# Kernel optimization log

Measured on AMD Instinct MI355X. Metric: run time of the kernel, lower is better.

The kernel has to match this reference:

```python
import jax, jax.numpy as jnp
import numpy as np


def setup_inputs() -> dict:
    key = jax.random.key(0)
    kq, ks, kr, kx, ky = jax.random.split(key, 5)
    B, C, H, W, K = 2, 64, 128, 256, 32
    Q = jax.random.normal(kq, (B, C, H, W), dtype=jnp.float32)
    S = jax.random.normal(ks, (B, C, H, W), dtype=jnp.float32)
    R = jax.random.normal(kr, (B, C, H, W), dtype=jnp.float32)
    Pos_x = jax.random.randint(kx, (H * W, K), 0, H, dtype=jnp.int64 if jax.config.jax_enable_x64 else jnp.int32)
    Pos_y = jax.random.randint(ky, (H * W, K), 0, W, dtype=jnp.int64 if jax.config.jax_enable_x64 else jnp.int32)
    return {"Q": Q, "S": S, "R": R, "Pos_x": Pos_x, "Pos_y": Pos_y}


def reference(Q, S, R, Pos_x, Pos_y):
    B, C, H, W = Q.shape
    N = H * W
    px = Pos_x.reshape(-1)  # [N*K]
    py = Pos_y.reshape(-1)
    K = px.shape[0] // N
    # Gather keys/values at candidate positions: [B, C, N*K] -> [B, C, N, K]
    Key = S[:, :, px, py].reshape(B, C, N, K)
    Value = R[:, :, px, py].reshape(B, C, N, K)
    # Queries: [B, N, C]
    Qf = Q.reshape(B, C, N).transpose(0, 2, 1)
    # Per-pixel scores over K candidates (NO 1/sqrt(d) scaling, as in original)
    score = jnp.einsum('bnc,bcnk->bnk', Qf, Key)
    attn = jax.nn.softmax(score, axis=-1)
    # Attention-weighted sum of values: [B, N, C]
    out = jnp.einsum('bnk,bcnk->bnc', attn, Value)
    return out.reshape(B, H, W, C).transpose(0, 3, 1, 2)
```

## Files before the change

### kernel.cpp

```cpp
#include <hip/hip_runtime.h>
#include <hip/hip_fp16.h>

constexpr int B = 2, C = 64, H = 128, W = 256, N = H * W, K = 32;

typedef _Float16 hf2 __attribute__((ext_vector_type(2)));

template <int CTRL>
__device__ __forceinline__ float dppf(float x) {
    int i = __builtin_bit_cast(int, x);
    int r = __builtin_amdgcn_update_dpp(i, i, CTRL, 0xF, 0xF, false);
    return __builtin_bit_cast(float, r);
}

__device__ __forceinline__ unsigned sel4(const ushort4& v, int g) {
    return g == 0 ? v.x : g == 1 ? v.y : g == 2 ? v.z : v.w;
}

__global__ __launch_bounds__(256) void fepam_prep(
    const float* __restrict__ Q, const float* __restrict__ S,
    const float* __restrict__ R,
    const int* __restrict__ Px, const int* __restrict__ Py,
    __half* __restrict__ Qt, __half* __restrict__ St, __half* __restrict__ Rt,
    unsigned short* __restrict__ Idx) {
    const int n0 = blockIdx.x * 64;
    const int b  = blockIdx.y;
    const int z  = blockIdx.z;

    if (z == 3) {
        if (b) return;
#pragma unroll
        for (int t = 0; t < 8; ++t) {
            const int e  = threadIdx.x + 256 * t;
            const int nl = e >> 5, k = e & 31;
            const int n  = n0 + nl;
            const int idx = Px[(size_t)n * K + k] * W + Py[(size_t)n * K + k];
            Idx[(size_t)n * K + (k & 7) * 4 + (k >> 3)] = (unsigned short)idx;
        }
        return;
    }

    __shared__ float tile[C][65];
    const float* src = (z == 0 ? S : (z == 1 ? R : Q)) + (size_t)b * C * N;
    __half2* d2 = (__half2*)((z == 0 ? St : (z == 1 ? Rt : Qt)) +
                             (size_t)b * N * C);
    {
        const int j = threadIdx.x & 63, c0 = threadIdx.x >> 6;
        const float* s = src + n0 + j;
#pragma unroll
        for (int r = 0; r < 16; ++r) {
            int c = c0 + r * 4;
            tile[c][j] = s[(size_t)c * N];
        }
    }
    __syncthreads();
    {
        const int c2 = threadIdx.x & 31, j0 = threadIdx.x >> 5;
#pragma unroll
        for (int r = 0; r < 8; ++r) {
            int j = j0 + 8 * r;
            d2[(size_t)(n0 + j) * 32 + c2] =
                __floats2half2_rn(tile[2 * c2][j], tile[2 * c2 + 1][j]);
        }
    }
}

__global__ __launch_bounds__(256, 6) void fepam_attn(
    const __half* __restrict__ Qt, const unsigned short* __restrict__ Idx,
    const __half* __restrict__ St, const __half* __restrict__ Rt,
    float* __restrict__ Out) {
    __shared__ __align__(16) float aw[32][32];
    __shared__ __align__(16) float ot[32][66];

    const int tid  = threadIdx.x;
    const int lane = tid & 63;
    const int wave = tid >> 6;
    const int bx   = blockIdx.x;
    const int b    = bx & 1;
    const int n0t  = (bx >> 1) * 32;
    const int n0   = n0t + wave * 8;

    const int c_oct = lane & 7;
    const int k_loc = lane >> 3;

    const __half* Qtb = Qt + (size_t)b * N * C;
    const __half* Stb = St + (size_t)b * N * C;
    const __half* Rtb = Rt + (size_t)b * N * C;

    auto ldi = [&](int p) {
        return *(const ushort4*)(Idx + (size_t)(n0 + p) * K + k_loc * 4);
    };

    {
        auto ldq = [&](int p) {
            return *(const float4*)(Qtb + (size_t)(n0 + p) * C + c_oct * 8);
        };
        auto ldk = [&](const ushort4& iv, int g) {
            return *(const float4*)(Stb + ((size_t)sel4(iv, g) << 6) +
                                    c_oct * 8);
        };

        ushort4 iv_c = ldi(0), iv_n = ldi(1);
        float4  q_c  = ldq(0), q_n  = ldq(1);
        float4  k_c[4];
#pragma unroll
        for (int g = 0; g < 4; ++g) k_c[g] = ldk(iv_c, g);

#pragma unroll
        for (int p = 0; p < 8; ++p) {
            float4 k_n[4];
            if (p < 7) {
#pragma unroll
                for (int g = 0; g < 4; ++g) k_n[g] = ldk(iv_n, g);
            }
            ushort4 iv_2;
            float4  q_2;
            if (p < 6) { iv_2 = ldi(p + 2); q_2 = ldq(p + 2); }

            float s[4];
#pragma unroll
            for (int g = 0; g < 4; ++g) {
                const hf2* k2 = (const hf2*)&k_c[g];
                const hf2* q2 = (const hf2*)&q_c;
                float acc = 0.f;
#pragma unroll
                for (int u = 0; u < 4; ++u)
                    acc = __builtin_amdgcn_fdot2(k2[u], q2[u], acc, false);
                s[g] = acc;
            }
#pragma unroll
            for (int g = 0; g < 4; ++g) {
                s[g] += dppf<0xB1>(s[g]);
                s[g] += dppf<0x4E>(s[g]);
                s[g] += dppf<0x141>(s[g]);
            }
            float m = fmaxf(fmaxf(s[0], s[1]), fmaxf(s[2], s[3]));
            m = fmaxf(m, dppf<0x128>(m));
            m = fmaxf(m, __shfl_xor(m, 16));
            m = fmaxf(m, __shfl_xor(m, 32));
            float e0 = __expf(s[0] - m), e1 = __expf(s[1] - m);
            float e2 = __expf(s[2] - m), e3 = __expf(s[3] - m);
            float l = (e0 + e1) + (e2 + e3);
            l += dppf<0x128>(l);
            l += __shfl_xor(l, 16);
            l += __shfl_xor(l, 32);
            const float inv = 1.0f / l;

            if (c_oct == 0) {
                *(float4*)&aw[wave * 8 + p][k_loc * 4] =
                    make_float4(e0 * inv, e1 * inv, e2 * inv, e3 * inv);
            }

#pragma unroll
            for (int g = 0; g < 4; ++g) k_c[g] = k_n[g];
            iv_c = iv_n; q_c = q_n;
            iv_n = iv_2; q_n = q_2;
        }
    }

    {
        const bool hi8  = (lane & 8)  != 0;
        const bool hi16 = (lane & 16) != 0;
        const bool hi32 = (lane & 32) != 0;

        auto ldv = [&](const ushort4& iv, int g) {
            return *(const float4*)(Rtb + ((size_t)sel4(iv, g) << 6) +
                                    c_oct * 8);
        };

        ushort4 i_c = ldi(0), i_n = ldi(1);
        float4  v_c[4];
#pragma unroll
        for (int g = 0; g < 4; ++g) v_c[g] = ldv(i_c, g);

#pragma unroll
        for (int p = 0; p < 8; ++p) {
            float4 v_n[4];
            if (p < 7) {
#pragma unroll
                for (int g = 0; g < 4; ++g) v_n[g] = ldv(i_n, g);
            }
            ushort4 i_2;
            if (p < 6) i_2 = ldi(p + 2);

            const float4 af = *(const float4*)&aw[wave * 8 + p][k_loc * 4];
            const float a[4] = {af.x, af.y, af.z, af.w};
            float acc[8] = {0, 0, 0, 0, 0, 0, 0, 0};
#pragma unroll
            for (int g = 0; g < 4; ++g) {
                const __half2* v2 = (const __half2*)&v_c[g];
#pragma unroll
                for (int u = 0; u < 4; ++u) {
                    const float2 vf = __half22float2(v2[u]);
                    acc[2 * u]     = fmaf(a[g], vf.x, acc[2 * u]);
                    acc[2 * u + 1] = fmaf(a[g], vf.y, acc[2 * u + 1]);
                }
            }

            float r4[4];
#pragma unroll
            for (int i = 0; i < 4; ++i) {
                const float send = hi8 ? acc[i] : acc[4 + i];
                const float recv = dppf<0x128>(send);
                r4[i] = (hi8 ? acc[4 + i] : acc[i]) + recv;
            }
            float r2[2];
#pragma unroll
            for (int i = 0; i < 2; ++i) {
                const float send = hi16 ? r4[i] : r4[2 + i];
                const float recv = __shfl_xor(send, 16);
                r2[i] = (hi16 ? r4[2 + i] : r4[i]) + recv;
            }
            {
                const float send = hi32 ? r2[0] : r2[1];
                const float recv = __shfl_xor(send, 32);
                const float r1   = (hi32 ? r2[1] : r2[0]) + recv;
                const int c = c_oct * 8 + (hi8 ? 4 : 0) + (hi16 ? 2 : 0) +
                              (hi32 ? 1 : 0);
                ot[wave * 8 + p][c] = r1;
            }

#pragma unroll
            for (int g = 0; g < 4; ++g) v_c[g] = v_n[g];
            i_c = i_n;
            i_n = i_2;
        }
    }
    __syncthreads();

    {
        const int j = tid & 31, c0 = tid >> 5;
        float* od = Out + (size_t)b * C * N + n0t + j;
#pragma unroll
        for (int r = 0; r < 8; ++r) {
            int c = c0 + r * 8;
            od[(size_t)c * N] = ot[j][c];
        }
    }
}

extern "C" void kernel_launch(void* const* d_in, const int* in_sizes, int n_in,
                              void* d_out, int out_size, void* d_ws, size_t ws_size,
                              hipStream_t stream) {
    const float* Q  = (const float*)d_in[0];
    const float* S  = (const float*)d_in[1];
    const float* R  = (const float*)d_in[2];
    const int*   Px = (const int*)d_in[3];
    const int*   Py = (const int*)d_in[4];
    float* Out = (float*)d_out;

    __half* St = (__half*)d_ws;
    __half* Rt = St + (size_t)B * N * C;
    __half* Qt = Rt + (size_t)B * N * C;
    unsigned short* Idx = (unsigned short*)(Qt + (size_t)B * N * C);

    dim3 pgrid(N / 64, B, 4);
    fepam_prep<<<pgrid, 256, 0, stream>>>(Q, S, R, Px, Py, Qt, St, Rt, Idx);

    dim3 ggrid(N / 32 * B);
    fepam_attn<<<ggrid, 256, 0, stream>>>(Qt, Idx, St, Rt, Out);
}
```

Before: 142.7 us.

## Split attention kernel into separate score and value-gather kernels

Splits the fused attention kernel into two launches. The first gathers keys and computes softmax weights, which it writes to a global fp16 buffer. The second gathers values and applies those weights. Each kernel touches only one gathered tensor (S or R), so the L2/MALL working set per phase is smaller and cache hit rates for the random gathers may improve. The cost is an extra launch, a global round trip for the weights (2*N*K fp16), and fp16 rounding of the attention weights.

Result: faster. 136.0 us (-4.7%).

```diff
diff --git a/kernel.cpp b/kernel.cpp
--- a/kernel.cpp
+++ b/kernel.cpp
@@ -64,11 +64,98 @@
     }
 }
 
-__global__ __launch_bounds__(256, 6) void fepam_attn(
+__global__ __launch_bounds__(256, 6) void fepam_scores(
     const __half* __restrict__ Qt, const unsigned short* __restrict__ Idx,
-    const __half* __restrict__ St, const __half* __restrict__ Rt,
-    float* __restrict__ Out) {
-    __shared__ __align__(16) float aw[32][32];
+    const __half* __restrict__ St, __half* __restrict__ AW) {
+    const int tid  = threadIdx.x;
+    const int lane = tid & 63;
+    const int wave = tid >> 6;
+    const int bx   = blockIdx.x;
+    const int b    = bx & 1;
+    const int n0   = (bx >> 1) * 32 + wave * 8;
+
+    const int c_oct = lane & 7;
+    const int k_loc = lane >> 3;
+
+    const __half* Qtb = Qt + (size_t)b * N * C;
+    const __half* Stb = St + (size_t)b * N * C;
+    __half* AWb = AW + (size_t)b * N * K;
+
+    auto ldi = [&](int p) {
+        return *(const ushort4*)(Idx + (size_t)(n0 + p) * K + k_loc * 4);
+    };
+    auto ldq = [&](int p) {
+        return *(const float4*)(Qtb + (size_t)(n0 + p) * C + c_oct * 8);
+    };
+    auto ldk = [&](const ushort4& iv, int g) {
+        return *(const float4*)(Stb + ((size_t)sel4(iv, g) << 6) + c_oct * 8);
+    };
+
+    ushort4 iv_c = ldi(0), iv_n = ldi(1);
+    float4  q_c  = ldq(0), q_n  = ldq(1);
+    float4  k_c[4];
+#pragma unroll
+    for (int g = 0; g < 4; ++g) k_c[g] = ldk(iv_c, g);
+
+#pragma unroll
+    for (int p = 0; p < 8; ++p) {
+        float4 k_n[4];
+        if (p < 7) {
+#pragma unroll
+            for (int g = 0; g < 4; ++g) k_n[g] = ldk(iv_n, g);
+        }
+        ushort4 iv_2;
+        float4  q_2;
+        if (p < 6) { iv_2 = ldi(p + 2); q_2 = ldq(p + 2); }
+
+        float s[4];
+#pragma unroll
+        for (int g = 0; g < 4; ++g) {
+            const hf2* k2 = (const hf2*)&k_c[g];
+            const hf2* q2 = (const hf2*)&q_c;
+            float acc = 0.f;
+#pragma unroll
+            for (int u = 0; u < 4; ++u)
+                acc = __builtin_amdgcn_fdot2(k2[u], q2[u], acc, false);
+            s[g] = acc;
+        }
+#pragma unroll
+        for (int g = 0; g < 4; ++g) {
+            s[g] += dppf<0xB1>(s[g]);
+            s[g] += dppf<0x4E>(s[g]);
+            s[g] += dppf<0x141>(s[g]);
+        }
+        float m = fmaxf(fmaxf(s[0], s[1]), fmaxf(s[2], s[3]));
+        m = fmaxf(m, dppf<0x128>(m));
+        m = fmaxf(m, __shfl_xor(m, 16));
+        m = fmaxf(m, __shfl_xor(m, 32));
+        float e0 = __expf(s[0] - m), e1 = __expf(s[1] - m);
+        float e2 = __expf(s[2] - m), e3 = __expf(s[3] - m);
+        float l = (e0 + e1) + (e2 + e3);
+        l += dppf<0x128>(l);
+        l += __shfl_xor(l, 16);
+        l += __shfl_xor(l, 32);
+        const float inv = 1.0f / l;
+
+        if (c_oct == 0) {
+            ushort4 hv;
+            hv.x = __half_as_ushort(__float2half_rn(e0 * inv));
+            hv.y = __half_as_ushort(__float2half_rn(e1 * inv));
+            hv.z = __half_as_ushort(__float2half_rn(e2 * inv));
+            hv.w = __half_as_ushort(__float2half_rn(e3 * inv));
+            *(ushort4*)(AWb + (size_t)(n0 + p) * K + k_loc * 4) = hv;
+        }
+
+#pragma unroll
+        for (int g = 0; g < 4; ++g) k_c[g] = k_n[g];
+        iv_c = iv_n; q_c = q_n;
+        iv_n = iv_2; q_n = q_2;
+    }
+}
+
+__global__ __launch_bounds__(256, 6) void fepam_values(
+    const unsigned short* __restrict__ Idx, const __half* __restrict__ AW,
+    const __half* __restrict__ Rt, float* __restrict__ Out) {
     __shared__ __align__(16) float ot[32][66];
 
     const int tid  = threadIdx.x;
@@ -81,149 +168,82 @@
 
     const int c_oct = lane & 7;
     const int k_loc = lane >> 3;
-
-    const __half* Qtb = Qt + (size_t)b * N * C;
-    const __half* Stb = St + (size_t)b * N * C;
+    const bool hi8  = (lane & 8)  != 0;
+    const bool hi16 = (lane & 16) != 0;
+    const bool hi32 = (lane & 32) != 0;
+
     const __half* Rtb = Rt + (size_t)b * N * C;
+    const __half* AWb = AW + (size_t)b * N * K;
 
     auto ldi = [&](int p) {
         return *(const ushort4*)(Idx + (size_t)(n0 + p) * K + k_loc * 4);
     };
-
-    {
-        auto ldq = [&](int p) {
-            return *(const float4*)(Qtb + (size_t)(n0 + p) * C + c_oct * 8);
-        };
-        auto ldk = [&](const ushort4& iv, int g) {
-            return *(const float4*)(Stb + ((size_t)sel4(iv, g) << 6) +
-                                    c_oct * 8);
-        };
-
-        ushort4 iv_c = ldi(0), iv_n = ldi(1);
-        float4  q_c  = ldq(0), q_n  = ldq(1);
-        float4  k_c[4];
-#pragma unroll
-        for (int g = 0; g < 4; ++g) k_c[g] = ldk(iv_c, g);
-
-#pragma unroll
-        for (int p = 0; p < 8; ++p) {
-            float4 k_n[4];
-            if (p < 7) {
-#pragma unroll
-                for (int g = 0; g < 4; ++g) k_n[g] = ldk(iv_n, g);
+    auto lda = [&](int p) {
+        return *(const ushort4*)(AWb + (size_t)(n0 + p) * K + k_loc * 4);
+    };
+    auto ldv = [&](const ushort4& iv, int g) {
+        return *(const float4*)(Rtb + ((size_t)sel4(iv, g) << 6) + c_oct * 8);
+    };
+
+    ushort4 i_c = ldi(0), i_n = ldi(1);
+    ushort4 a_c = lda(0), a_n = lda(1);
+    float4  v_c[4];
+#pragma unroll
+    for (int g = 0; g < 4; ++g) v_c[g] = ldv(i_c, g);
+
+#pragma unroll
+    for (int p = 0; p < 8; ++p) {
+        float4 v_n[4];
+        if (p < 7) {
+#pragma unroll
+            for (int g = 0; g < 4; ++g) v_n[g] = ldv(i_n, g);
+        }
+        ushort4 i_2, a_2;
+        if (p < 6) { i_2 = ldi(p + 2); a_2 = lda(p + 2); }
+
+        const float a[4] = {
+            __half2float(__ushort_as_half(a_c.x)),
+            __half2float(__ushort_as_half(a_c.y)),
+            __half2float(__ushort_as_half(a_c.z)),
+            __half2float(__ushort_as_half(a_c.w))};
+        float acc[8] = {0, 0, 0, 0, 0, 0, 0, 0};
+#pragma unroll
+        for (int g = 0; g < 4; ++g) {
+            const __half2* v2 = (const __half2*)&v_c[g];
+#pragma unroll
+            for (int u = 0; u < 4; ++u) {
+                const float2 vf = __half22float2(v2[u]);
+                acc[2 * u]     = fmaf(a[g], vf.x, acc[2 * u]);
+                acc[2 * u + 1] = fmaf(a[g], vf.y, acc[2 * u + 1]);
             }
-            ushort4 iv_2;
-            float4  q_2;
-            if (p < 6) { iv_2 = ldi(p + 2); q_2 = ldq(p + 2); }
-
-            float s[4];
-#pragma unroll
-            for (int g = 0; g < 4; ++g) {
-                const hf2* k2 = (const hf2*)&k_c[g];
-                const hf2* q2 = (const hf2*)&q_c;
-                float acc = 0.f;
-#pragma unroll
-                for (int u = 0; u < 4; ++u)
-                    acc = __builtin_amdgcn_fdot2(k2[u], q2[u], acc, false);
-                s[g] = acc;
-            }
-#pragma unroll
-            for (int g = 0; g < 4; ++g) {
-                s[g] += dppf<0xB1>(s[g]);
-                s[g] += dppf<0x4E>(s[g]);
-                s[g] += dppf<0x141>(s[g]);
-            }
-            float m = fmaxf(fmaxf(s[0], s[1]), fmaxf(s[2], s[3]));
-            m = fmaxf(m, dppf<0x128>(m));
-            m = fmaxf(m, __shfl_xor(m, 16));
-            m = fmaxf(m, __shfl_xor(m, 32));
-            float e0 = __expf(s[0] - m), e1 = __expf(s[1] - m);
-            float e2 = __expf(s[2] - m), e3 = __expf(s[3] - m);
-            float l = (e0 + e1) + (e2 + e3);
-            l += dppf<0x128>(l);
-            l += __shfl_xor(l, 16);
-            l += __shfl_xor(l, 32);
-            const float inv = 1.0f / l;
-
-            if (c_oct == 0) {
-                *(float4*)&aw[wave * 8 + p][k_loc * 4] =
-                    make_float4(e0 * inv, e1 * inv, e2 * inv, e3 * inv);
-            }
-
-#pragma unroll
-            for (int g = 0; g < 4; ++g) k_c[g] = k_n[g];
-            iv_c = iv_n; q_c = q_n;
-            iv_n = iv_2; q_n = q_2;
-        }
-    }
-
-    {
-        const bool hi8  = (lane & 8)  != 0;
-        const bool hi16 = (lane & 16) != 0;
-        const bool hi32 = (lane & 32) != 0;
-
-        auto ldv = [&](const ushort4& iv, int g) {
-            return *(const float4*)(Rtb + ((size_t)sel4(iv, g) << 6) +
-                                    c_oct * 8);
-        };
-
-        ushort4 i_c = ldi(0), i_n = ldi(1);
-        float4  v_c[4];
-#pragma unroll
-        for (int g = 0; g < 4; ++g) v_c[g] = ldv(i_c, g);
-
-#pragma unroll
-        for (int p = 0; p < 8; ++p) {
-            float4 v_n[4];
-            if (p < 7) {
-#pragma unroll
-                for (int g = 0; g < 4; ++g) v_n[g] = ldv(i_n, g);
-            }
-            ushort4 i_2;
-            if (p < 6) i_2 = ldi(p + 2);
-
-            const float4 af = *(const float4*)&aw[wave * 8 + p][k_loc * 4];
-            const float a[4] = {af.x, af.y, af.z, af.w};
-            float acc[8] = {0, 0, 0, 0, 0, 0, 0, 0};
-#pragma unroll
-            for (int g = 0; g < 4; ++g) {
-                const __half2* v2 = (const __half2*)&v_c[g];
-#pragma unroll
-                for (int u = 0; u < 4; ++u) {
-                    const float2 vf = __half22float2(v2[u]);
-                    acc[2 * u]     = fmaf(a[g], vf.x, acc[2 * u]);
-                    acc[2 * u + 1] = fmaf(a[g], vf.y, acc[2 * u + 1]);
-                }
-            }
-
-            float r4[4];
-#pragma unroll
-            for (int i = 0; i < 4; ++i) {
-                const float send = hi8 ? acc[i] : acc[4 + i];
-                const float recv = dppf<0x128>(send);
-                r4[i] = (hi8 ? acc[4 + i] : acc[i]) + recv;
-            }
-            float r2[2];
-#pragma unroll
-            for (int i = 0; i < 2; ++i) {
-                const float send = hi16 ? r4[i] : r4[2 + i];
-                const float recv = __shfl_xor(send, 16);
-                r2[i] = (hi16 ? r4[2 + i] : r4[i]) + recv;
-            }
-            {
-                const float send = hi32 ? r2[0] : r2[1];
-                const float recv = __shfl_xor(send, 32);
-                const float r1   = (hi32 ? r2[1] : r2[0]) + recv;
-                const int c = c_oct * 8 + (hi8 ? 4 : 0) + (hi16 ? 2 : 0) +
-                              (hi32 ? 1 : 0);
-                ot[wave * 8 + p][c] = r1;
-            }
-
-#pragma unroll
-            for (int g = 0; g < 4; ++g) v_c[g] = v_n[g];
-            i_c = i_n;
-            i_n = i_2;
-        }
+        }
+
+        float r4[4];
+#pragma unroll
+        for (int i = 0; i < 4; ++i) {
+            const float send = hi8 ? acc[i] : acc[4 + i];
+            const float recv = dppf<0x128>(send);
+            r4[i] = (hi8 ? acc[4 + i] : acc[i]) + recv;
+        }
+        float r2[2];
+#pragma unroll
+        for (int i = 0; i < 2; ++i) {
+            const float send = hi16 ? r4[i] : r4[2 + i];
+            const float recv = __shfl_xor(send, 16);
+            r2[i] = (hi16 ? r4[2 + i] : r4[i]) + recv;
+        }
+        {
+            const float send = hi32 ? r2[0] : r2[1];
+            const float recv = __shfl_xor(send, 32);
+            const float r1   = (hi32 ? r2[1] : r2[0]) + recv;
+            const int c = c_oct * 8 + (hi8 ? 4 : 0) + (hi16 ? 2 : 0) + (hi32 ? 1 : 0);
+            ot[wave * 8 + p][c] = r1;
+        }
+
+#pragma unroll
+        for (int g = 0; g < 4; ++g) v_c[g] = v_n[g];
+        i_c = i_n; a_c = a_n;
+        i_n = i_2; a_n = a_2;
     }
     __syncthreads();
 
@@ -252,10 +272,12 @@
     __half* Rt = St + (size_t)B * N * C;
     __half* Qt = Rt + (size_t)B * N * C;
     unsigned short* Idx = (unsigned short*)(Qt + (size_t)B * N * C);
+    __half* AW = (__half*)(Idx + (size_t)N * K);
 
     dim3 pgrid(N / 64, B, 4);
     fepam_prep<<<pgrid, 256, 0, stream>>>(Q, S, R, Px, Py, Qt, St, Rt, Idx);
 
     dim3 ggrid(N / 32 * B);
-    fepam_attn<<<ggrid, 256, 0, stream>>>(Qt, Idx, St, Rt, Out);
-}
+    fepam_scores<<<ggrid, 256, 0, stream>>>(Qt, Idx, St, AW);
+    fepam_values<<<ggrid, 256, 0, stream>>>(Idx, AW, Rt, Out);
+}
```
